# Performance work log

Measured on AMD Instinct MI355X. Metric: run time of the kernel, lower is better.

The kernel has to match this reference:

```python
import jax, jax.numpy as jnp
import numpy as np

B, T, C = 2, 4096, 2048
HS = 64
DW, DA, DV, DG = 128, 128, 64, 224


def setup_inputs() -> dict:
    key = jax.random.key(0)
    ks = jax.random.split(key, 32)
    s = 0.02  # small weight scale to keep activations in a sane range
    inp = {
        'x': jax.random.normal(ks[0], (B, T, C), jnp.float32),
        'v_first': jax.random.normal(ks[1], (B, T, C), jnp.float32),
        'x_r': jax.random.uniform(ks[2], (C,), jnp.float32),
        'x_w': jax.random.uniform(ks[3], (C,), jnp.float32),
        'x_k': jax.random.uniform(ks[4], (C,), jnp.float32),
        'x_v': jax.random.uniform(ks[5], (C,), jnp.float32),
        'x_a': jax.random.uniform(ks[6], (C,), jnp.float32),
        'x_g': jax.random.uniform(ks[7], (C,), jnp.float32),
        'w0': jax.random.normal(ks[8], (C,), jnp.float32),
        'w1': jax.random.normal(ks[9], (C, DW), jnp.float32) * s,
        'w2': jax.random.normal(ks[10], (DW, C), jnp.float32) * s,
        'a0': jax.random.normal(ks[11], (C,), jnp.float32),
        'a1': jax.random.normal(ks[12], (C, DA), jnp.float32) * s,
        'a2': jax.random.normal(ks[13], (DA, C), jnp.float32) * s,
        'v0': jax.random.normal(ks[14], (C,), jnp.float32),
        'v1': jax.random.normal(ks[15], (C, DV), jnp.float32) * s,
        'v2': jax.random.normal(ks[16], (DV, C), jnp.float32) * s,
        'g1': jax.random.normal(ks[17], (C, DG), jnp.float32) * s,
        'g2': jax.random.normal(ks[18], (DG, C), jnp.float32) * s,
        'k_k': jax.random.normal(ks[19], (C,), jnp.float32) * 0.1 + 0.71,
        'k_a': jnp.full((C,), 1.02, jnp.float32),
        'Wr': jax.random.normal(ks[20], (C, C), jnp.float32) * s,
        'Wk': jax.random.normal(ks[21], (C, C), jnp.float32) * s,
        'Wv': jax.random.normal(ks[22], (C, C), jnp.float32) * s,
        'head_size': HS,
    }
    return inp


def reference(x, v_first, x_r, x_w, x_k, x_v, x_a, x_g,
              w0, w1, w2, a0, a1, a2, v0, v1, v2, g1, g2,
              k_k, k_a, Wr, Wk, Wv, head_size):
    Bd, Td, Cd = x.shape
    H = Cd // head_size
    # time shift: prepend zero frame, drop last
    xprev = jnp.concatenate([jnp.zeros_like(x[:, :1]), x[:, :-1]], axis=1)
    xx = xprev - x
    xr = x + xx * x_r
    xw = x + xx * x_w
    xk = x + xx * x_k
    xv = x + xx * x_v
    xa = x + xx * x_a
    xg = x + xx * x_g
    r = xr @ Wr.T                                   # [B,T,C]
    w = -jax.nn.softplus(-(w0 + jnp.tanh(xw @ w1) @ w2)) - 0.5
    k = xk @ Wk.T
    v = xv @ Wv.T
    # layer_id = 1 != 0  ->  mix with v_first
    v = v + (v_first - v) * jax.nn.sigmoid(v0 + (xv @ v1) @ v2)
    a = jax.nn.sigmoid(a0 + (xa @ a1) @ a2)
    g = jax.nn.sigmoid(xg @ g1) @ g2
    kk = k * k_k
    kk4 = kk.reshape(Bd, Td, H, head_size)
    nrm = jnp.linalg.norm(kk4, axis=-1, keepdims=True)
    kk = (kk4 / jnp.maximum(nrm, 1e-12)).reshape(Bd, Td, Cd)
    k = k * (1.0 + (a - 1.0) * k_a)
    return (r, w, k, v, a, g, kk, v_first)
```

## Files before the change

### kernel.cpp

```cpp
#include <hip/hip_runtime.h>
#include <hip/hip_bf16.h>

#define MTOT 8192
#define TLEN 4096
#define CDIM 2048
#define SLOT ((size_t)MTOT * CDIM)

typedef __attribute__((ext_vector_type(4))) float f32x4;
typedef __attribute__((ext_vector_type(8))) __bf16 bf16x8;

__device__ __forceinline__ short f2bf(float f) {
  __hip_bfloat16 h = __float2bfloat16(f);
  return __builtin_bit_cast(short, h);
}

__device__ __forceinline__ float sigm(float x) { return 1.f / (1.f + expf(-x)); }

__device__ __forceinline__ void gload16(const void* g, void* l) {
  __builtin_amdgcn_global_load_lds(
      (__attribute__((address_space(1))) void*)g,
      (__attribute__((address_space(3))) void*)l, 16, 0, 0);
}

__device__ __forceinline__ void gemm_core(
    int tid,
    const short* __restrict__ A, int lda,
    const short* __restrict__ Bt, int ldb,
    int K, int m0, int n0,
    short* As, short* Bs, f32x4 acc[4][4])
{
  const int lane = tid & 63;
  const int wv   = tid >> 6;
  const int wy   = wv >> 1;
  const int wx   = wv & 1;
  const int quad = lane >> 4;
  const int m16  = lane & 15;

  const f32x4 zero = {0.f, 0.f, 0.f, 0.f};
  #pragma unroll
  for (int i = 0; i < 4; ++i)
    #pragma unroll
    for (int j = 0; j < 4; ++j)
      acc[i][j] = zero;

  const int e0 = (wv * 64 + lane) * 8;
  const int e1 = e0 + 2048;
  const int r0 = e0 >> 5, c0 = e0 & 31;
  const int r1 = e1 >> 5, c1 = e1 & 31;
  const int lb0 = wv * 512;
  const int lb1 = 2048 + wv * 512;

  const short* pa0 = A  + (size_t)(m0 + r0) * lda + c0;
  const short* pa1 = A  + (size_t)(m0 + r1) * lda + c1;
  const short* pb0 = Bt + (size_t)(n0 + r0) * ldb + c0;
  const short* pb1 = Bt + (size_t)(n0 + r1) * ldb + c1;

  for (int k0 = 0; k0 < K; k0 += 32) {
    gload16(pa0 + k0, As + lb0);
    gload16(pa1 + k0, As + lb1);
    gload16(pb0 + k0, Bs + lb0);
    gload16(pb1 + k0, Bs + lb1);
    __syncthreads();

    bf16x8 af[4], bfr[4];
    #pragma unroll
    for (int mi = 0; mi < 4; ++mi)
      af[mi] = *(const bf16x8*)(As + (wy*64 + mi*16 + m16)*32 + quad*8);
    #pragma unroll
    for (int ni = 0; ni < 4; ++ni)
      bfr[ni] = *(const bf16x8*)(Bs + (wx*64 + ni*16 + m16)*32 + quad*8);

    #pragma unroll
    for (int mi = 0; mi < 4; ++mi)
      #pragma unroll
      for (int ni = 0; ni < 4; ++ni)
        acc[mi][ni] = __builtin_amdgcn_mfma_f32_16x16x32_bf16(
            af[mi], bfr[ni], acc[mi][ni], 0, 0, 0);
    __syncthreads();
  }
}

__global__ __launch_bounds__(256) void front(
    const float* __restrict__ x, const float* __restrict__ vfin,
    const float* __restrict__ cr, const float* __restrict__ cw,
    const float* __restrict__ ck, const float* __restrict__ cv,
    const float* __restrict__ ca, const float* __restrict__ cg,
    const float* __restrict__ Wr, const float* __restrict__ Wk,
    const float* __restrict__ Wv,
    const float* __restrict__ w1, const float* __restrict__ a1,
    const float* __restrict__ v1, const float* __restrict__ g1,
    const float* __restrict__ w2, const float* __restrict__ a2,
    const float* __restrict__ v2, const float* __restrict__ g2,
    short* __restrict__ xr, short* __restrict__ xw, short* __restrict__ xk,
    short* __restrict__ xv, short* __restrict__ xa, short* __restrict__ xg,
    float* __restrict__ vfout,
    short* __restrict__ Wrb, short* __restrict__ Wkb, short* __restrict__ Wvb,
    short* __restrict__ w1t, short* __restrict__ a1t,
    short* __restrict__ v1t, short* __restrict__ g1t,
    short* __restrict__ w2t, short* __restrict__ a2t,
    short* __restrict__ v2t, short* __restrict__ g2t)
{
  const int b = blockIdx.x;
  const int tidx = threadIdx.x;

  if (b < 16384) {
    const size_t i = (size_t)b * 256 + tidx;
    const size_t e = i * 4;
    const int c = (int)(e & (CDIM - 1));
    const size_t m = e >> 11;
    const int t = (int)(m & (TLEN - 1));
    const float4 xc = *(const float4*)(x + e);
    float4 xp = make_float4(0.f, 0.f, 0.f, 0.f);
    if (t > 0) xp = *(const float4*)(x + e - CDIM);
    const float d0 = xp.x - xc.x, d1 = xp.y - xc.y;
    const float d2 = xp.z - xc.z, d3 = xp.w - xc.w;

    *(float4*)(vfout + e) = *(const float4*)(vfin + e);

    #define EMIT(coef, dst) { \
      const float4 cf = *(const float4*)((coef) + c); \
      short4 s; \
      s.x = f2bf(xc.x + d0 * cf.x); \
      s.y = f2bf(xc.y + d1 * cf.y); \
      s.z = f2bf(xc.z + d2 * cf.z); \
      s.w = f2bf(xc.w + d3 * cf.w); \
      *(short4*)((dst) + e) = s; }
    EMIT(cr, xr) EMIT(cw, xw) EMIT(ck, xk) EMIT(cv, xv) EMIT(ca, xa) EMIT(cg, xg)
    #undef EMIT
  } else if (b < 28672) {
    const int lb = b - 16384;
    const int z = lb >> 12;
    const int xb = lb & 4095;
    const float* src = (z == 0) ? Wr : (z == 1) ? Wk : Wv;
    short* dst = (z == 0) ? Wrb : (z == 1) ? Wkb : Wvb;
    const size_t e = ((size_t)xb * 256 + tidx) * 4;
    const float4 v = *(const float4*)(src + e);
    short4 s;
    s.x = f2bf(v.x); s.y = f2bf(v.y); s.z = f2bf(v.z); s.w = f2bf(v.w);
    *(short4*)(dst + e) = s;
  } else {
    const int lb = b - 28672;
    const int task = lb >> 11;
    const int i = (lb & 2047) * 256 + tidx;
    switch (task) {
      case 0: if (i < 128*2048) { int d=i>>11, c=i&2047; w1t[i]=f2bf(w1[(size_t)c*128+d]); } break;
      case 1: if (i < 128*2048) { int d=i>>11, c=i&2047; a1t[i]=f2bf(a1[(size_t)c*128+d]); } break;
      case 2: if (i < 128*2048) { int d=i>>11, c=i&2047; v1t[i]=(d<64)?f2bf(v1[(size_t)c*64+d]):(short)0; } break;
      case 3: if (i < 256*2048) { int d=i>>11, c=i&2047; g1t[i]=(d<224)?f2bf(g1[(size_t)c*224+d]):(short)0; } break;
      case 4: if (i < 2048*128) { int c=i>>7, d=i&127; w2t[i]=f2bf(w2[(size_t)d*2048+c]); } break;
      case 5: if (i < 2048*128) { int c=i>>7, d=i&127; a2t[i]=f2bf(a2[(size_t)d*2048+c]); } break;
      case 6: if (i < 2048*64)  { int c=i>>6, d=i&63;  v2t[i]=f2bf(v2[(size_t)d*2048+c]); } break;
      case 7: if (i < 2048*224) { int c=i/224, d=i-c*224; g2t[i]=f2bf(g2[(size_t)d*2048+c]); } break;
    }
  }
}

__global__ __launch_bounds__(512, 2) void gemm_big2(
    const short* __restrict__ xr, const short* __restrict__ xk,
    const short* __restrict__ xv,
    const short* __restrict__ Wr, const short* __restrict__ Wk,
    const short* __restrict__ Wv,
    const short* __restrict__ xw, const short* __restrict__ xa,
    const short* __restrict__ xg,
    const short* __restrict__ w1t, const short* __restrict__ a1t,
    const short* __restrict__ v1t, const short* __restrict__ g1t,
    short* __restrict__ hw, short* __restrict__ ha,
    short* __restrict__ hv, short* __restrict__ hg,
    float* __restrict__ out)
{
  __shared__ short As[32768];
  __shared__ short Bs[32768];

  const int z = blockIdx.z;

  if (z == 3) {
    const int flat = blockIdx.x + (blockIdx.y << 5);
    if (flat >= 160) return;
    const int sub = threadIdx.x >> 8;
    const int tid = threadIdx.x & 255;
    const int tile = flat * 2 + sub;
    const int t = tile >> 6;
    const int mt = tile & 63;
    const short* A1 = (t==0) ? xw  : (t==1) ? xa  : (t==2) ? xv  : xg;
    const short* B1 = (t==0) ? w1t : (t==1) ? a1t : (t==2) ? v1t : g1t;
    short* H        = (t==0) ? hw  : (t==1) ? ha  : (t==2) ? hv  : hg;
    const int Nreal = (t==2) ? 64 : (t>=3) ? 224 : 128;
    const int n0 = (t==4) ? 128 : 0;
    const int m0 = mt * 128;
    short* sA = As + sub * 8192;
    short* sB = sA + 4096;
    f32x4 acc[4][4];
    gemm_core(tid, A1, CDIM, B1, CDIM, CDIM, m0, n0, sA, sB, acc);

    const int lane=tid&63, wv=tid>>6;
    const int wy=wv>>1, wx=wv&1, quad=lane>>4, m16=lane&15;
    #pragma unroll
    for (int mi = 0; mi < 4; ++mi) {
      const int mb = m0 + wy*64 + mi*16 + quad*4;
      #pragma unroll
      for (int ni = 0; ni < 4; ++ni) {
        const int n = n0 + wx*64 + ni*16 + m16;
        if (n < Nreal) {
          #pragma unroll
          for (int r = 0; r < 4; ++r) {
            float v = acc[mi][ni][r];
            if (t == 0) v = tanhf(v);
            else if (t >= 3) v = sigm(v);
            H[(size_t)(mb + r) * Nreal + n] = f2bf(v);
          }
        }
      }
    }
    return;
  }

  const short* A  = (z == 0) ? xr : (z == 1) ? xk : xv;
  const short* Bt = (z == 0) ? Wr : (z == 1) ? Wk : Wv;
  float* O = (z == 0) ? out : (z == 1) ? out + 2*SLOT : out + 3*SLOT;

  const int flat = blockIdx.x + (blockIdx.y << 5);
  const int m0 = (flat >> 3) * 256;
  const int n0 = (flat & 7)  * 256;
  const int tid  = threadIdx.x;
  const int lane = tid & 63, wid = tid >> 6;
  const int wm = wid >> 2, wn = wid & 3;
  const int quad = lane >> 4, m16 = lane & 15;

  const int srow = tid >> 2;
  const int csrc = (((tid & 3) ^ ((tid >> 3) & 3)) << 3);
  const size_t aoff = (size_t)(m0 + srow) * CDIM + csrc;
  const size_t boff = (size_t)(n0 + srow) * CDIM + csrc;
  const int lbase = wid * 512;

  const int fslot = ((quad ^ ((m16 >> 1) & 3)) << 3);
  const int abase = (wm*128 + m16) * 32 + fslot;
  const int bbase = (wn*64  + m16) * 32 + fslot;

  f32x4 acc[8][4];
  const f32x4 zf = {0.f, 0.f, 0.f, 0.f};
  #pragma unroll
  for (int i = 0; i < 8; ++i)
    #pragma unroll
    for (int j = 0; j < 4; ++j) acc[i][j] = zf;

  #define STG(REG, BASEP, OFF, KOFF) do { \
    gload16((BASEP) + (OFF) + (KOFF), (REG) + lbase); \
    gload16((BASEP) + (OFF) + (KOFF) + (size_t)128*CDIM, (REG) + lbase + 4096); \
  } while (0)

  STG(As + 0,    A,  aoff, 0);
  STG(Bs + 0,    Bt, boff, 0);
  STG(As + 8192, A,  aoff, 32);
  STG(Bs + 8192, Bt, boff, 32);
  asm volatile("s_waitcnt vmcnt(4)" ::: "memory");
  __builtin_amdgcn_s_barrier();
  __builtin_amdgcn_sched_barrier(0);

  const int NT = CDIM / 64;
  for (int t = 0; t < NT; ++t) {
    const int db = (t & 1) << 14;
    const int nb = 16384 - db;
    const int kn = t*64 + 64;
    const bool pf = (kn < CDIM);
    short* Ar0 = As + db;
    short* Br0 = Bs + db;
    short* Ar1 = As + db + 8192;
    short* Br1 = Bs + db + 8192;

    bf16x8 af[8], b0, b1, b2, b3;

    #pragma unroll
    for (int mi = 0; mi < 8; ++mi)
      af[mi] = *(const bf16x8*)(Ar0 + abase + mi*512);
    b0 = *(const bf16x8*)(Br0 + bbase + 0*512);
    b1 = *(const bf16x8*)(Br0 + bbase + 1*512);
    b2 = *(const bf16x8*)(Br0 + bbase + 2*512);
    b3 = *(const bf16x8*)(Br0 + bbase + 3*512);
    if (pf) STG(As + nb, A, aoff, kn);
    __builtin_amdgcn_s_barrier();
    asm volatile("s_waitcnt lgkmcnt(0)" ::: "memory");
    __builtin_amdgcn_sched_barrier(0);
    __builtin_amdgcn_s_setprio(1);
    #pragma unroll
    for (int mi = 0; mi < 8; ++mi)
      acc[mi][0] = __builtin_amdgcn_mfma_f32_16x16x32_bf16(af[mi], b0, acc[mi][0], 0, 0, 0);
    #pragma unroll
    for (int mi = 0; mi < 8; ++mi)
      acc[mi][1] = __builtin_amdgcn_mfma_f32_16x16x32_bf16(af[mi], b1, acc[mi][1], 0, 0, 0);
    __builtin_amdgcn_s_setprio(0);
    __builtin_amdgcn_s_barrier();

    if (pf) STG(Bs + nb, Bt, boff, kn);
    __builtin_amdgcn_s_barrier();
    __builtin_amdgcn_s_setprio(1);
    #pragma unroll
    for (int mi = 0; mi < 8; ++mi)
      acc[mi][2] = __builtin_amdgcn_mfma_f32_16x16x32_bf16(af[mi], b2, acc[mi][2], 0, 0, 0);
    #pragma unroll
    for (int mi = 0; mi < 8; ++mi)
      acc[mi][3] = __builtin_amdgcn_mfma_f32_16x16x32_bf16(af[mi], b3, acc[mi][3], 0, 0, 0);
    __builtin_amdgcn_s_setprio(0);
    if (pf) asm volatile("s_waitcnt vmcnt(4)" ::: "memory");
    else    asm volatile("s_waitcnt vmcnt(0)" ::: "memory");
    __builtin_amdgcn_s_barrier();
    __builtin_amdgcn_sched_barrier(0);

    #pragma unroll
    for (int mi = 0; mi < 8; ++mi)
      af[mi] = *(const bf16x8*)(Ar1 + abase + mi*512);
    b0 = *(const bf16x8*)(Br1 + bbase + 0*512);
    b1 = *(const bf16x8*)(Br1 + bbase + 1*512);
    b2 = *(const bf16x8*)(Br1 + bbase + 2*512);
    b3 = *(const bf16x8*)(Br1 + bbase + 3*512);
    if (pf) STG(As + nb + 8192, A, aoff, kn + 32);
    __builtin_amdgcn_s_barrier();
    asm volatile("s_waitcnt lgkmcnt(0)" ::: "memory");
    __builtin_amdgcn_sched_barrier(0);
    __builtin_amdgcn_s_setprio(1);
    #pragma unroll
    for (int mi = 0; mi < 8; ++mi)
      acc[mi][0] = __builtin_amdgcn_mfma_f32_16x16x32_bf16(af[mi], b0, acc[mi][0], 0, 0, 0);
    #pragma unroll
    for (int mi = 0; mi < 8; ++mi)
      acc[mi][1] = __builtin_amdgcn_mfma_f32_16x16x32_bf16(af[mi], b1, acc[mi][1], 0, 0, 0);
    __builtin_amdgcn_s_setprio(0);
    __builtin_amdgcn_s_barrier();

    if (pf) STG(Bs + nb + 8192, Bt, boff, kn + 32);
    __builtin_amdgcn_s_barrier();
    __builtin_amdgcn_s_setprio(1);
    #pragma unroll
    for (int mi = 0; mi < 8; ++mi)
      acc[mi][2] = __builtin_amdgcn_mfma_f32_16x16x32_bf16(af[mi], b2, acc[mi][2], 0, 0, 0);
    #pragma unroll
    for (int mi = 0; mi < 8; ++mi)
      acc[mi][3] = __builtin_amdgcn_mfma_f32_16x16x32_bf16(af[mi], b3, acc[mi][3], 0, 0, 0);
    __builtin_amdgcn_s_setprio(0);
    asm volatile("s_waitcnt vmcnt(4)" ::: "memory");
    __builtin_amdgcn_s_barrier();
    __builtin_amdgcn_sched_barrier(0);
  }
  #undef STG

  #pragma unroll
  for (int mi = 0; mi < 8; ++mi) {
    const int row = m0 + wm*128 + mi*16 + quad*4;
    #pragma unroll
    for (int ni = 0; ni < 4; ++ni) {
      const int col = n0 + wn*64 + ni*16 + m16;
      #pragma unroll
      for (int r = 0; r < 4; ++r)
        O[(size_t)(row + r) * CDIM + col] = acc[mi][ni][r];
    }
  }
}

__global__ __launch_bounds__(256) void gemm_s2(
    const short* __restrict__ hw, const short* __restrict__ ha,
    const short* __restrict__ hv, const short* __restrict__ hg,
    const short* __restrict__ w2t, const short* __restrict__ a2t,
    const short* __restrict__ v2t, const short* __restrict__ g2t,
    const float* __restrict__ w0, const float* __restrict__ a0,
    const float* __restrict__ v0, const float* __restrict__ vfirst,
    const float* __restrict__ kkc, const float* __restrict__ kac,
    float* __restrict__ out)
{
  __shared__ short As[4096], Bs[4096];
  const int z = blockIdx.z;
  const short* A  = (z==0) ? hw  : (z==1) ? ha  : (z==2) ? hv  : hg;
  const short* Bt = (z==0) ? w2t : (z==1) ? a2t : (z==2) ? v2t : g2t;
  const int K = (z==2) ? 64 : (z==3) ? 224 : 128;
  const int m0 = blockIdx.x * 128, n0 = blockIdx.y * 128;
  f32x4 acc[4][4];
  gemm_core(threadIdx.x, A, K, Bt, K, K, m0, n0, As, Bs, acc);

  const int tid=threadIdx.x, lane=tid&63, wv=tid>>6;
  const int wy=wv>>1, wx=wv&1, quad=lane>>4, m16=lane&15;
  #pragma unroll
  for (int mi = 0; mi < 4; ++mi) {
    const int mb = m0 + wy*64 + mi*16 + quad*4;
    if (z == 1) {
      #pragma unroll
      for (int r = 0; r < 4; ++r) {
        float av[4], kr[4], kkv[4];
        float ss = 0.f;
        #pragma unroll
        for (int ni = 0; ni < 4; ++ni) {
          const int n = n0 + wx*64 + ni*16 + m16;
          const size_t idx = (size_t)(mb + r) * CDIM + n;
          av[ni] = sigm(a0[n] + acc[mi][ni][r]);
          kr[ni] = out[2*SLOT + idx];
          kkv[ni] = kr[ni] * kkc[n];
          ss += kkv[ni] * kkv[ni];
        }
        ss += __shfl_xor(ss, 1, 64);
        ss += __shfl_xor(ss, 2, 64);
        ss += __shfl_xor(ss, 4, 64);
        ss += __shfl_xor(ss, 8, 64);
        const float inv = 1.f / fmaxf(sqrtf(ss), 1e-12f);
        #pragma unroll
        for (int ni = 0; ni < 4; ++ni) {
          const int n = n0 + wx*64 + ni*16 + m16;
          const size_t idx = (size_t)(mb + r) * CDIM + n;
          out[4*SLOT + idx] = av[ni];
          out[2*SLOT + idx] = kr[ni] * (1.f + (av[ni] - 1.f) * kac[n]);
          out[6*SLOT + idx] = kkv[ni] * inv;
        }
      }
    } else {
      #pragma unroll
      for (int ni = 0; ni < 4; ++ni) {
        const int n = n0 + wx*64 + ni*16 + m16;
        #pragma unroll
        for (int r = 0; r < 4; ++r) {
          const float val = acc[mi][ni][r];
          const size_t idx = (size_t)(mb + r) * CDIM + n;
          if (z == 0) {
            float zz = w0[n] + val;
            float sp = fmaxf(-zz, 0.f) + log1pf(expf(-fabsf(zz)));
            out[SLOT + idx] = -sp - 0.5f;
          } else if (z == 2) {
            const float gate = sigm(v0[n] + val);
            const float vr = out[3*SLOT + idx];
            out[3*SLOT + idx] = vr + (vfirst[idx] - vr) * gate;
          } else {
            out[5*SLOT + idx] = val;
          }
        }
      }
    }
  }
}

extern "C" void kernel_launch(void* const* d_in, const int* in_sizes, int n_in,
                              void* d_out, int out_size, void* d_ws, size_t ws_size,
                              hipStream_t stream) {
  (void)in_sizes; (void)n_in; (void)out_size; (void)ws_size;
  const float* x   = (const float*)d_in[0];
  const float* vf  = (const float*)d_in[1];
  const float* x_r = (const float*)d_in[2];
  const float* x_w = (const float*)d_in[3];
  const float* x_k = (const float*)d_in[4];
  const float* x_v = (const float*)d_in[5];
  const float* x_a = (const float*)d_in[6];
  const float* x_g = (const float*)d_in[7];
  const float* w0  = (const float*)d_in[8];
  const float* w1  = (const float*)d_in[9];
  const float* w2  = (const float*)d_in[10];
  const float* a0  = (const float*)d_in[11];
  const float* a1  = (const float*)d_in[12];
  const float* a2  = (const float*)d_in[13];
  const float* v0  = (const float*)d_in[14];
  const float* v1  = (const float*)d_in[15];
  const float* v2  = (const float*)d_in[16];
  const float* g1  = (const float*)d_in[17];
  const float* g2  = (const float*)d_in[18];
  const float* k_k = (const float*)d_in[19];
  const float* k_a = (const float*)d_in[20];
  const float* Wr  = (const float*)d_in[21];
  const float* Wk  = (const float*)d_in[22];
  const float* Wv  = (const float*)d_in[23];

  float* out = (float*)d_out;

  short* xr_b = (short*)(out + 1*SLOT);
  short* xw_b = xr_b + SLOT;
  short* xk_b = (short*)(out + 4*SLOT);
  short* xv_b = xk_b + SLOT;
  short* xa_b = (short*)(out + 5*SLOT);
  short* xg_b = xa_b + SLOT;

  char* wsp = (char*)d_ws;
  size_t off = 0;
  #define ALLOC(var, bytes) short* var = (short*)(wsp + off); off += (((size_t)(bytes)) + 255) & ~(size_t)255;
  ALLOC(Wr_b, (size_t)CDIM*CDIM*2)
  ALLOC(Wk_b, (size_t)CDIM*CDIM*2)
  ALLOC(Wv_b, (size_t)CDIM*CDIM*2)
  ALLOC(w1t, 128*2048*2)
  ALLOC(a1t, 128*2048*2)
  ALLOC(v1t, 128*2048*2)
  ALLOC(g1t, 256*2048*2)
  ALLOC(w2t, 2048*128*2)
  ALLOC(a2t, 2048*128*2)
  ALLOC(v2t, 2048*64*2)
  ALLOC(g2t, 2048*224*2)
  ALLOC(hw, (size_t)MTOT*128*2)
  ALLOC(ha, (size_t)MTOT*128*2)
  ALLOC(hv, (size_t)MTOT*64*2)
  ALLOC(hg, (size_t)MTOT*224*2)
  #undef ALLOC

  front<<<dim3(45056), 256, 0, stream>>>(
      x, vf, x_r, x_w, x_k, x_v, x_a, x_g,
      Wr, Wk, Wv, w1, a1, v1, g1, w2, a2, v2, g2,
      xr_b, xw_b, xk_b, xv_b, xa_b, xg_b, out + 7*SLOT,
      Wr_b, Wk_b, Wv_b, w1t, a1t, v1t, g1t, w2t, a2t, v2t, g2t);

  gemm_big2<<<dim3(32, 8, 4), 512, 0, stream>>>(
      xr_b, xk_b, xv_b, Wr_b, Wk_b, Wv_b,
      xw_b, xa_b, xg_b, w1t, a1t, v1t, g1t,
      hw, ha, hv, hg, out);

  gemm_s2<<<dim3(64, 16, 4), 256, 0, stream>>>(
      hw, ha, hv, hg, w2t, a2t, v2t, g2t, w0, a0, v0, vf, k_k, k_a, out);
}
```

Baseline: 1.246 ms.

## Double-buffer gemm_core K loop, fuse v_first copy into epilogue, nontemporal stores

The small-GEMM core now double-buffers its LDS tiles and prefetches two K-steps ahead, using vmcnt waits and raw barriers in place of a load-sync-compute-sync loop. The v_first passthrough copy moves out of the front kernel into the gemm_s2 z==2 epilogue, which already reads vfirst, so v_first is read from HBM once instead of twice. Output stores in the epilogues become nontemporal to keep streaming writes from polluting cache. The cost is doubled LDS per block for gemm_s2 and for the z==3 path in gemm_big2, which may lower occupancy.

```diff
diff --git a/kernel.cpp b/kernel.cpp
--- a/kernel.cpp
+++ b/kernel.cpp
@@ -15,6 +15,10 @@
 }
 
 __device__ __forceinline__ float sigm(float x) { return 1.f / (1.f + expf(-x)); }
+
+__device__ __forceinline__ void stnt(float* p, float v) {
+  __builtin_nontemporal_store(v, p);
+}
 
 __device__ __forceinline__ void gload16(const void* g, void* l) {
   __builtin_amdgcn_global_load_lds(
@@ -55,20 +59,31 @@
   const short* pb0 = Bt + (size_t)(n0 + r0) * ldb + c0;
   const short* pb1 = Bt + (size_t)(n0 + r1) * ldb + c1;
 
-  for (int k0 = 0; k0 < K; k0 += 32) {
-    gload16(pa0 + k0, As + lb0);
-    gload16(pa1 + k0, As + lb1);
-    gload16(pb0 + k0, Bs + lb0);
-    gload16(pb1 + k0, Bs + lb1);
-    __syncthreads();
+  const int NTk = K >> 5;
+
+  #define STG1(T, BUF) do { const int kk_ = (T) * 32; \
+    gload16(pa0 + kk_, As + (BUF)*4096 + lb0); \
+    gload16(pa1 + kk_, As + (BUF)*4096 + lb1); \
+    gload16(pb0 + kk_, Bs + (BUF)*4096 + lb0); \
+    gload16(pb1 + kk_, Bs + (BUF)*4096 + lb1); } while (0)
+
+  STG1(0, 0);
+  if (NTk > 1) STG1(1, 1);
+
+  for (int t = 0; t < NTk; ++t) {
+    const int buf = (t & 1) * 4096;
+    if (t + 1 < NTk) asm volatile("s_waitcnt vmcnt(4)" ::: "memory");
+    else             asm volatile("s_waitcnt vmcnt(0)" ::: "memory");
+    __builtin_amdgcn_s_barrier();
+    __builtin_amdgcn_sched_barrier(0);
 
     bf16x8 af[4], bfr[4];
     #pragma unroll
     for (int mi = 0; mi < 4; ++mi)
-      af[mi] = *(const bf16x8*)(As + (wy*64 + mi*16 + m16)*32 + quad*8);
+      af[mi] = *(const bf16x8*)(As + buf + (wy*64 + mi*16 + m16)*32 + quad*8);
     #pragma unroll
     for (int ni = 0; ni < 4; ++ni)
-      bfr[ni] = *(const bf16x8*)(Bs + (wx*64 + ni*16 + m16)*32 + quad*8);
+      bfr[ni] = *(const bf16x8*)(Bs + buf + (wx*64 + ni*16 + m16)*32 + quad*8);
 
     #pragma unroll
     for (int mi = 0; mi < 4; ++mi)
@@ -76,12 +91,16 @@
       for (int ni = 0; ni < 4; ++ni)
         acc[mi][ni] = __builtin_amdgcn_mfma_f32_16x16x32_bf16(
             af[mi], bfr[ni], acc[mi][ni], 0, 0, 0);
-    __syncthreads();
+
+    __builtin_amdgcn_s_barrier();
+    __builtin_amdgcn_sched_barrier(0);
+    if (t + 2 < NTk) STG1(t + 2, buf == 0 ? 0 : 1);
   }
+  #undef STG1
 }
 
 __global__ __launch_bounds__(256) void front(
-    const float* __restrict__ x, const float* __restrict__ vfin,
+    const float* __restrict__ x,
     const float* __restrict__ cr, const float* __restrict__ cw,
     const float* __restrict__ ck, const float* __restrict__ cv,
     const float* __restrict__ ca, const float* __restrict__ cg,
@@ -93,7 +112,6 @@
     const float* __restrict__ v2, const float* __restrict__ g2,
     short* __restrict__ xr, short* __restrict__ xw, short* __restrict__ xk,
     short* __restrict__ xv, short* __restrict__ xa, short* __restrict__ xg,
-    float* __restrict__ vfout,
     short* __restrict__ Wrb, short* __restrict__ Wkb, short* __restrict__ Wvb,
     short* __restrict__ w1t, short* __restrict__ a1t,
     short* __restrict__ v1t, short* __restrict__ g1t,
@@ -114,8 +132,6 @@
     if (t > 0) xp = *(const float4*)(x + e - CDIM);
     const float d0 = xp.x - xc.x, d1 = xp.y - xc.y;
     const float d2 = xp.z - xc.z, d3 = xp.w - xc.w;
-
-    *(float4*)(vfout + e) = *(const float4*)(vfin + e);
 
     #define EMIT(coef, dst) { \
       const float4 cf = *(const float4*)((coef) + c); \
@@ -188,7 +204,7 @@
     const int n0 = (t==4) ? 128 : 0;
     const int m0 = mt * 128;
     short* sA = As + sub * 8192;
-    short* sB = sA + 4096;
+    short* sB = Bs + sub * 8192;
     f32x4 acc[4][4];
     gemm_core(tid, A1, CDIM, B1, CDIM, CDIM, m0, n0, sA, sB, acc);
 
@@ -349,8 +365,11 @@
     for (int ni = 0; ni < 4; ++ni) {
       const int col = n0 + wn*64 + ni*16 + m16;
       #pragma unroll
-      for (int r = 0; r < 4; ++r)
-        O[(size_t)(row + r) * CDIM + col] = acc[mi][ni][r];
+      for (int r = 0; r < 4; ++r) {
+        float* p = O + (size_t)(row + r) * CDIM + col;
+        if (z == 0) stnt(p, acc[mi][ni][r]);
+        else        *p = acc[mi][ni][r];
+      }
     }
   }
 }
@@ -365,7 +384,7 @@
     const float* __restrict__ kkc, const float* __restrict__ kac,
     float* __restrict__ out)
 {
-  __shared__ short As[4096], Bs[4096];
+  __shared__ short As[8192], Bs[8192];
   const int z = blockIdx.z;
   const short* A  = (z==0) ? hw  : (z==1) ? ha  : (z==2) ? hv  : hg;
   const short* Bt = (z==0) ? w2t : (z==1) ? a2t : (z==2) ? v2t : g2t;
@@ -402,9 +421,9 @@
         for (int ni = 0; ni < 4; ++ni) {
           const int n = n0 + wx*64 + ni*16 + m16;
           const size_t idx = (size_t)(mb + r) * CDIM + n;
-          out[4*SLOT + idx] = av[ni];
-          out[2*SLOT + idx] = kr[ni] * (1.f + (av[ni] - 1.f) * kac[n]);
-          out[6*SLOT + idx] = kkv[ni] * inv;
+          stnt(out + 4*SLOT + idx, av[ni]);
+          stnt(out + 2*SLOT + idx, kr[ni] * (1.f + (av[ni] - 1.f) * kac[n]));
+          stnt(out + 6*SLOT + idx, kkv[ni] * inv);
         }
       }
     } else {
@@ -418,13 +437,15 @@
           if (z == 0) {
             float zz = w0[n] + val;
             float sp = fmaxf(-zz, 0.f) + log1pf(expf(-fabsf(zz)));
-            out[SLOT + idx] = -sp - 0.5f;
+            stnt(out + SLOT + idx, -sp - 0.5f);
           } else if (z == 2) {
+            const float vfv = vfirst[idx];
             const float gate = sigm(v0[n] + val);
             const float vr = out[3*SLOT + idx];
-            out[3*SLOT + idx] = vr + (vfirst[idx] - vr) * gate;
+            stnt(out + 3*SLOT + idx, vr + (vfv - vr) * gate);
+            stnt(out + 7*SLOT + idx, vfv);
           } else {
-            out[5*SLOT + idx] = val;
+            stnt(out + 5*SLOT + idx, val);
           }
         }
       }
@@ -491,9 +512,9 @@
   #undef ALLOC
 
   front<<<dim3(45056), 256, 0, stream>>>(
-      x, vf, x_r, x_w, x_k, x_v, x_a, x_g,
+      x, x_r, x_w, x_k, x_v, x_a, x_g,
       Wr, Wk, Wv, w1, a1, v1, g1, w2, a2, v2, g2,
-      xr_b, xw_b, xk_b, xv_b, xa_b, xg_b, out + 7*SLOT,
+      xr_b, xw_b, xk_b, xv_b, xa_b, xg_b,
       Wr_b, Wk_b, Wv_b, w1t, a1t, v1t, g1t, w2t, a2t, v2t, g2t);
 
   gemm_big2<<<dim3(32, 8, 4), 512, 0, stream>>>(
```

New measurement: 1.228 ms. No clear change (-1.4%).
